# Optimization experiments

Measured on AMD Instinct MI355X. Metric: run time of the kernel, lower is better.

The kernel has to match this reference:

```python
import jax, jax.numpy as jnp
import numpy as np

N = 50000   # nodes
E = 800000  # edges (avg degree 16)
D = 256     # input = hidden = output dim
L = 3       # num_layers


def setup_inputs() -> dict:
    key = jax.random.key(0)
    k0, k1, k2, k3 = jax.random.split(key, 4)
    x = jax.random.normal(k0, (N, D), dtype=jnp.float32)
    edge_index = jax.random.randint(k1, (2, E), 0, N, dtype=jnp.int32)
    # SAGEConv params per layer: lin_l (neighbor path, with bias), lin_r (root path)
    Wl = jax.random.normal(k2, (L, D, D), dtype=jnp.float32) * 0.05
    Wr = jax.random.normal(k3, (L, D, D), dtype=jnp.float32) * 0.05
    b = jnp.zeros((L, D), dtype=jnp.float32)
    return {"x": x, "edge_index": edge_index, "Wl": Wl, "Wr": Wr, "b": b}


def reference(x, edge_index, Wl, Wr, b):
    src = edge_index[0]
    dst = edge_index[1]
    # in-degree for mean aggregation (clamped to avoid div-by-zero)
    deg = jax.ops.segment_sum(jnp.ones((E,), x.dtype), dst, num_segments=N)
    inv_deg = (1.0 / jnp.maximum(deg, 1.0))[:, None]  # [N,1]
    h = x
    for i in range(L):
        # gather source features, scatter-add into destinations, then mean
        agg = jax.ops.segment_sum(h[src], dst, num_segments=N) * inv_deg  # [N,D]
        h = agg @ Wl[i] + h @ Wr[i] + b[i]
        if i < L - 1:
            h = jax.nn.relu(h)  # dropout(p=0.1) is identity in eval mode
    return h
```

## Files before the change

### kernel.cpp

```cpp
#include <hip/hip_runtime.h>


typedef __attribute__((ext_vector_type(8))) _Float16 f16x8;
typedef __attribute__((ext_vector_type(4))) float f32x4;

__global__ void count_deg_kernel(const int* __restrict__ dst,
                                 int* __restrict__ deg, int E) {
    int i = (blockIdx.x * blockDim.x + threadIdx.x) * 2;
    if (i + 1 < E) {
        int2 d = *(const int2*)&dst[i];
        atomicAdd(&deg[d.x], 1);
        atomicAdd(&deg[d.y], 1);
    } else if (i < E) {
        atomicAdd(&deg[dst[i]], 1);
    }
}

__device__ __forceinline__ int block_excl_scan_256(int v, int tid) {
    int lane = tid & 63, w = tid >> 6;
    int x = v;
#pragma unroll
    for (int off = 1; off < 64; off <<= 1) {
        int y = __shfl_up(x, off);
        if (lane >= off) x += y;
    }
    __shared__ int wsum[4], woff[4];
    if (lane == 63) wsum[w] = x;
    __syncthreads();
    if (tid == 0) {
        int a = 0;
#pragma unroll
        for (int i = 0; i < 4; ++i) { woff[i] = a; a += wsum[i]; }
    }
    __syncthreads();
    return woff[w] + x - v;
}

__global__ void scan_phase1(const int* __restrict__ deg,
                            int* __restrict__ partial, int n) {
    int base = blockIdx.x * 1024;
    int s = 0;
    for (int i = threadIdx.x; i < 1024; i += 256) {
        int idx = base + i;
        s += (idx < n) ? deg[idx] : 0;
    }
    __shared__ int ws4[4];
    int lane = threadIdx.x & 63, w = threadIdx.x >> 6;
#pragma unroll
    for (int off = 32; off; off >>= 1) s += __shfl_down(s, off);
    if (lane == 0) ws4[w] = s;
    __syncthreads();
    if (threadIdx.x == 0)
        partial[blockIdx.x] = ws4[0] + ws4[1] + ws4[2] + ws4[3];
}

__global__ void scan_phase2(int* __restrict__ partial, int nb,
                            int* __restrict__ rowptr, int n, int E) {
    int tid = threadIdx.x;
    int v = (tid < nb) ? partial[tid] : 0;
    int ex = block_excl_scan_256(v, tid);
    if (tid < nb) partial[tid] = ex;
    if (tid == 0) rowptr[n] = E;
}

__global__ void scan_phase3(const int* __restrict__ deg,
                            const int* __restrict__ partial,
                            int* __restrict__ rowptr, int* __restrict__ cursor,
                            float* __restrict__ inv_deg, int n) {
    int base = blockIdx.x * 1024 + threadIdx.x * 4;
    int d[4];
#pragma unroll
    for (int j = 0; j < 4; ++j) {
        int idx = base + j;
        d[j] = (idx < n) ? deg[idx] : 0;
    }
    int tsum = d[0] + d[1] + d[2] + d[3];
    int ex = block_excl_scan_256(tsum, threadIdx.x);
    int run = partial[blockIdx.x] + ex;
#pragma unroll
    for (int j = 0; j < 4; ++j) {
        int idx = base + j;
        if (idx < n) {
            rowptr[idx] = run;
            cursor[idx] = run;
            inv_deg[idx] = 1.0f / (float)max(d[j], 1);
        }
        run += d[j];
    }
}

__global__ void fill_csr_kernel(const int* __restrict__ src,
                                const int* __restrict__ dst,
                                int* __restrict__ cursor,
                                int* __restrict__ csr_src, int E) {
    int i = (blockIdx.x * blockDim.x + threadIdx.x) * 2;
    if (i + 1 < E) {
        int2 d = *(const int2*)&dst[i];
        int2 s = *(const int2*)&src[i];
        int p0 = atomicAdd(&cursor[d.x], 1);
        csr_src[p0] = s.x;
        int p1 = atomicAdd(&cursor[d.y], 1);
        csr_src[p1] = s.y;
    } else if (i < E) {
        int p = atomicAdd(&cursor[dst[i]], 1);
        csr_src[p] = src[i];
    }
}

__global__ void presplit_w_kernel(const float* __restrict__ Wl,
                                  const float* __restrict__ Wr,
                                  _Float16* __restrict__ Wf,
                                  int* __restrict__ deg, int N, int total) {
    int idx = blockIdx.x * blockDim.x + threadIdx.x;
    if (idx < N) deg[idx] = 0;
    if (idx >= total) return;
    int l = idx >> 17;
    int rem = idx & 131071;
    int s = rem >> 16;
    int kc = rem & 65535;
    int k = kc >> 8, c = kc & 255;
    const float* W = s ? Wr : Wl;
    float w = W[((size_t)l * 256 + k) * 256 + c];
    int k0c = k >> 5, g = (k >> 3) & 3, j = k & 7;
    int tile = c >> 4, col = c & 15;
    int fi = (l * 2 + s) * 65536 + k0c * 8192 + ((tile * 4 + g) * 16 + col) * 8 + j;
    Wf[fi] = (_Float16)w;
}

__device__ __forceinline__ void gemm_from_lds64(
    const _Float16 (*Ah)[65][8], int tid, const _Float16* __restrict__ Wf_l,
    const float* __restrict__ bias, _Float16* __restrict__ zl,
    _Float16* __restrict__ zr, int r0, int M) {
    const int wave = tid >> 6, lane = tid & 63;
    const int l15 = lane & 15, lg = lane >> 4;
    const int wr = (wave & 1) * 32;
    const int wc = (wave >> 1) * 64;
    const int tg0 = wc >> 4;
    const _Float16* wbase = Wf_l + (lg * 16 + l15) * 8;

    f32x4 accl[2][4], accr[2][4];
#pragma unroll
    for (int rt = 0; rt < 2; ++rt)
#pragma unroll
        for (int t = 0; t < 4; ++t) {
            accl[rt][t] = (f32x4)(0.0f);
            accr[rt][t] = (f32x4)(0.0f);
        }

    f16x8 blc[4], brc[4];
#pragma unroll
    for (int t = 0; t < 4; ++t) {
        blc[t] = *(const f16x8*)&wbase[(tg0 + t) * 512];
        brc[t] = *(const f16x8*)&wbase[65536 + (tg0 + t) * 512];
    }

#pragma unroll
    for (int s = 0; s < 8; ++s) {
        f16x8 bln[4], brn[4];
        if (s < 7) {
            const _Float16* wn = wbase + (s + 1) * 8192;
#pragma unroll
            for (int t = 0; t < 4; ++t) {
                bln[t] = *(const f16x8*)&wn[(tg0 + t) * 512];
                brn[t] = *(const f16x8*)&wn[65536 + (tg0 + t) * 512];
            }
        }
        f16x8 a0 = *(const f16x8*)&Ah[s * 4 + lg][wr + l15][0];
        f16x8 a1 = *(const f16x8*)&Ah[s * 4 + lg][wr + 16 + l15][0];
#pragma unroll
        for (int t = 0; t < 4; ++t) {
            accl[0][t] = __builtin_amdgcn_mfma_f32_16x16x32_f16(a0, blc[t],
                                                                accl[0][t], 0, 0, 0);
            accl[1][t] = __builtin_amdgcn_mfma_f32_16x16x32_f16(a1, blc[t],
                                                                accl[1][t], 0, 0, 0);
            accr[0][t] = __builtin_amdgcn_mfma_f32_16x16x32_f16(a0, brc[t],
                                                                accr[0][t], 0, 0, 0);
            accr[1][t] = __builtin_amdgcn_mfma_f32_16x16x32_f16(a1, brc[t],
                                                                accr[1][t], 0, 0, 0);
        }
        if (s < 7) {
#pragma unroll
            for (int t = 0; t < 4; ++t) {
                blc[t] = bln[t];
                brc[t] = brn[t];
            }
        }
    }

    float bv[4];
#pragma unroll
    for (int t = 0; t < 4; ++t) bv[t] = bias[wc + t * 16 + l15];
#pragma unroll
    for (int rt = 0; rt < 2; ++rt) {
#pragma unroll
        for (int r = 0; r < 4; ++r) {
            int grow = r0 + wr + rt * 16 + lg * 4 + r;
            if (grow >= M) continue;
#pragma unroll
            for (int t = 0; t < 4; ++t) {
                int col = wc + t * 16 + l15;
                int p = col >> 5, off = col & 31;
                size_t zi = ((size_t)p * M + grow) * 32 + off;
                zl[zi] = (_Float16)accl[rt][t][r];
                zr[zi] = (_Float16)(accr[rt][t][r] + bv[t]);
            }
        }
    }
}

__global__ __launch_bounds__(512) void gemm_dual_kernel(
    const float* __restrict__ xsrc, const _Float16* __restrict__ hsrc,
    int f32src, _Float16* __restrict__ zl, _Float16* __restrict__ zr,
    const _Float16* __restrict__ Wf_l, const float* __restrict__ bias, int M) {
    __shared__ __align__(16) _Float16 Ah[32][65][8];
    const int tid = threadIdx.x;
    const int r0 = blockIdx.x * 64;
#pragma unroll
    for (int i = 0; i < 4; ++i) {
        int idx = i * 512 + tid;
        int row = idx >> 5, g = idx & 31;
        int grow = r0 + row;
        f16x8 v = (f16x8)(_Float16)0;
        if (grow < M) {
            if (f32src) {
                const float4* p =
                    (const float4*)&xsrc[(size_t)grow * 256 + g * 8];
                float4 v0 = p[0], v1 = p[1];
                v[0] = (_Float16)v0.x; v[1] = (_Float16)v0.y;
                v[2] = (_Float16)v0.z; v[3] = (_Float16)v0.w;
                v[4] = (_Float16)v1.x; v[5] = (_Float16)v1.y;
                v[6] = (_Float16)v1.z; v[7] = (_Float16)v1.w;
            } else {
                v = *(const f16x8*)&hsrc[(size_t)grow * 256 + g * 8];
            }
        }
        *(f16x8*)&Ah[g][row][0] = v;
    }
    __syncthreads();
    gemm_from_lds64(Ah, tid, Wf_l, bias, zl, zr, r0, M);
}

__global__ __launch_bounds__(256) void combine_panel_kernel(
    const _Float16* __restrict__ zl, const _Float16* __restrict__ zr,
    const int* __restrict__ rowptr, const int* __restrict__ csr_src,
    const float* __restrict__ inv_deg, _Float16* __restrict__ hout,
    float* __restrict__ fout, int n, int mode) {
    const int slice = blockIdx.x & 7;
    const int chunk = blockIdx.x >> 3;
    const int grp = threadIdx.x >> 2;
    const int l4 = threadIdx.x & 3;
    const _Float16* zlp = zl + (size_t)slice * n * 32 + l4 * 8;
    const _Float16* zrp = zr + (size_t)slice * n * 32 + l4 * 8;

#pragma unroll
    for (int i = 0; i < 4; ++i) {
        int v = chunk * 256 + i * 64 + grp;
        if (v >= n) continue;
        int beg = rowptr[v], end = rowptr[v + 1];
        float acc[8] = {0.f, 0.f, 0.f, 0.f, 0.f, 0.f, 0.f, 0.f};
        for (int e = beg; e < end; e += 8) {
            f16x8 t[8];
#pragma unroll
            for (int k = 0; k < 8; ++k) {
                int ee = min(e + k, end - 1);
                int u = csr_src[ee];
                t[k] = *(const f16x8*)&zlp[(size_t)u * 32];
            }
#pragma unroll
            for (int k = 0; k < 8; ++k) {
                if (e + k < end) {
#pragma unroll
                    for (int j = 0; j < 8; ++j) acc[j] += (float)t[k][j];
                }
            }
        }
        float sc = inv_deg[v];
        f16x8 zp = *(const f16x8*)&zrp[(size_t)v * 32];
        float o[8];
#pragma unroll
        for (int j = 0; j < 8; ++j) o[j] = acc[j] * sc + (float)zp[j];
        int cbase = slice * 32 + l4 * 8;
        if (mode == 0) {
            f16x8 hv;
#pragma unroll
            for (int j = 0; j < 8; ++j) hv[j] = (_Float16)fmaxf(o[j], 0.0f);
            *(f16x8*)&hout[(size_t)v * 256 + cbase] = hv;
        } else {
            float4* op = (float4*)&fout[(size_t)v * 256 + cbase];
            op[0] = make_float4(o[0], o[1], o[2], o[3]);
            op[1] = make_float4(o[4], o[5], o[6], o[7]);
        }
    }
}

extern "C" void kernel_launch(void* const* d_in, const int* in_sizes, int n_in,
                              void* d_out, int out_size, void* d_ws, size_t ws_size,
                              hipStream_t stream) {
    const int D = 256;
    const int N = in_sizes[0] / D;
    const int E = in_sizes[1] / 2;
    const int L = in_sizes[2] / (D * D);

    const float* x  = (const float*)d_in[0];
    const int*   ei = (const int*)d_in[1];
    const float* Wl = (const float*)d_in[2];
    const float* Wr = (const float*)d_in[3];
    const float* b  = (const float*)d_in[4];
    const int* src = ei;
    const int* dst = ei + E;

    size_t off = 0;
    auto alloc = [&](size_t bytes) {
        void* p = (char*)d_ws + off;
        off += (bytes + 255) & ~(size_t)255;
        return p;
    };
    int*   deg     = (int*)alloc((size_t)N * 4);
    int*   rowptr  = (int*)alloc((size_t)(N + 1) * 4);
    int*   cursor  = (int*)alloc((size_t)N * 4);
    float* inv_deg = (float*)alloc((size_t)N * 4);
    int*   csr_src = (int*)alloc((size_t)E * 4);
    int*   partial = (int*)alloc(256 * 4);
    _Float16* zlP  = (_Float16*)alloc((size_t)N * D * 2);
    _Float16* zrP  = (_Float16*)alloc((size_t)N * D * 2);
    _Float16* hbuf = (_Float16*)alloc((size_t)N * D * 2);
    _Float16* Wf   = (_Float16*)alloc((size_t)L * 2 * 65536 * 2);
    (void)ws_size;

    _Float16* zlQ = (_Float16*)d_out;
    _Float16* zrQ = zlQ + (size_t)N * D;
    float* outf = (float*)d_out;

    const int scan_blocks = (N + 1023) / 1024;

    int wtotal = L * 2 * 65536;
    hipLaunchKernelGGL(presplit_w_kernel, dim3((wtotal + 255) / 256), dim3(256),
                       0, stream, Wl, Wr, Wf, deg, N, wtotal);

    hipLaunchKernelGGL(count_deg_kernel, dim3((E / 2 + 255) / 256), dim3(256),
                       0, stream, dst, deg, E);
    hipLaunchKernelGGL(scan_phase1, dim3(scan_blocks), dim3(256), 0, stream,
                       deg, partial, N);
    hipLaunchKernelGGL(scan_phase2, dim3(1), dim3(256), 0, stream,
                       partial, scan_blocks, rowptr, N, E);
    hipLaunchKernelGGL(scan_phase3, dim3(scan_blocks), dim3(256), 0, stream,
                       deg, partial, rowptr, cursor, inv_deg, N);
    hipLaunchKernelGGL(fill_csr_kernel, dim3((E / 2 + 255) / 256), dim3(256),
                       0, stream, src, dst, cursor, csr_src, E);

    const int gemm_blocks = (N + 63) / 64;
    const int comb_blocks = 8 * ((N + 255) / 256);

    hipLaunchKernelGGL(gemm_dual_kernel, dim3(gemm_blocks), dim3(512), 0,
                       stream, x, (const _Float16*)nullptr, 1, zlP, zrP,
                       Wf, b, N);
    hipLaunchKernelGGL(combine_panel_kernel, dim3(comb_blocks), dim3(256), 0,
                       stream, zlP, zrP, rowptr, csr_src, inv_deg,
                       hbuf, outf, N, 0);
    hipLaunchKernelGGL(gemm_dual_kernel, dim3(gemm_blocks), dim3(512), 0,
                       stream, (const float*)nullptr, hbuf, 0, zlQ, zrQ,
                       Wf + 131072, b + D, N);
    hipLaunchKernelGGL(combine_panel_kernel, dim3(comb_blocks), dim3(256), 0,
                       stream, zlQ, zrQ, rowptr, csr_src, inv_deg,
                       hbuf, outf, N, 0);
    hipLaunchKernelGGL(gemm_dual_kernel, dim3(gemm_blocks), dim3(512), 0,
                       stream, (const float*)nullptr, hbuf, 0, zlP, zrP,
                       Wf + 262144, b + 2 * D, N);
    hipLaunchKernelGGL(combine_panel_kernel, dim3(comb_blocks), dim3(256), 0,
                       stream, zlP, zrP, rowptr, csr_src, inv_deg,
                       hbuf, outf, N, 1);
}
```

Before: 391.6 us.

## Sort nodes by degree bucket for balanced aggregation and widen gather unroll

Adds a counting-sort pass (histogram, scan, scatter) that orders nodes by in-degree, and the combine kernel walks nodes through this permutation so neighbouring threads have similar degrees. This is meant to cut wavefront divergence from uneven neighbour loop trip counts. The gather unroll also grows from 8 to 16 outstanding loads per iteration for more memory-level parallelism. The cost is three extra small launches, an extra indirection, scattered output writes and more registers.

```diff
diff --git a/kernel.cpp b/kernel.cpp
--- a/kernel.cpp
+++ b/kernel.cpp
@@ -107,12 +107,43 @@
     }
 }
 
+__global__ void bucket_hist_kernel(const int* __restrict__ deg,
+                                   int* __restrict__ hist, int n) {
+    int i = blockIdx.x * blockDim.x + threadIdx.x;
+    if (i < n) atomicAdd(&hist[min(deg[i], 63)], 1);
+}
+
+__global__ void bucket_scan_kernel(int* __restrict__ hist) {
+    int tid = threadIdx.x;
+    int v = hist[tid];
+    int x = v;
+#pragma unroll
+    for (int off = 1; off < 64; off <<= 1) {
+        int y = __shfl_up(x, off);
+        if (tid >= off) x += y;
+    }
+    hist[tid] = x - v;
+}
+
+__global__ void bucket_scatter_kernel(const int* __restrict__ deg,
+                                      int* __restrict__ hist,
+                                      int* __restrict__ perm, int n) {
+    int i = blockIdx.x * blockDim.x + threadIdx.x;
+    if (i < n) {
+        int b = min(deg[i], 63);
+        int p = atomicAdd(&hist[b], 1);
+        perm[p] = i;
+    }
+}
+
 __global__ void presplit_w_kernel(const float* __restrict__ Wl,
                                   const float* __restrict__ Wr,
                                   _Float16* __restrict__ Wf,
-                                  int* __restrict__ deg, int N, int total) {
+                                  int* __restrict__ deg, int* __restrict__ hist,
+                                  int N, int total) {
     int idx = blockIdx.x * blockDim.x + threadIdx.x;
     if (idx < N) deg[idx] = 0;
+    if (idx < 64) hist[idx] = 0;
     if (idx >= total) return;
     int l = idx >> 17;
     int rem = idx & 131071;
@@ -243,8 +274,8 @@
 __global__ __launch_bounds__(256) void combine_panel_kernel(
     const _Float16* __restrict__ zl, const _Float16* __restrict__ zr,
     const int* __restrict__ rowptr, const int* __restrict__ csr_src,
-    const float* __restrict__ inv_deg, _Float16* __restrict__ hout,
-    float* __restrict__ fout, int n, int mode) {
+    const float* __restrict__ inv_deg, const int* __restrict__ perm,
+    _Float16* __restrict__ hout, float* __restrict__ fout, int n, int mode) {
     const int slice = blockIdx.x & 7;
     const int chunk = blockIdx.x >> 3;
     const int grp = threadIdx.x >> 2;
@@ -254,28 +285,29 @@
 
 #pragma unroll
     for (int i = 0; i < 4; ++i) {
-        int v = chunk * 256 + i * 64 + grp;
-        if (v >= n) continue;
+        int idx = chunk * 256 + i * 64 + grp;
+        if (idx >= n) continue;
+        int v = perm[idx];
         int beg = rowptr[v], end = rowptr[v + 1];
+        float sc = inv_deg[v];
+        f16x8 zp = *(const f16x8*)&zrp[(size_t)v * 32];
         float acc[8] = {0.f, 0.f, 0.f, 0.f, 0.f, 0.f, 0.f, 0.f};
-        for (int e = beg; e < end; e += 8) {
-            f16x8 t[8];
-#pragma unroll
-            for (int k = 0; k < 8; ++k) {
+        for (int e = beg; e < end; e += 16) {
+            f16x8 t[16];
+#pragma unroll
+            for (int k = 0; k < 16; ++k) {
                 int ee = min(e + k, end - 1);
                 int u = csr_src[ee];
                 t[k] = *(const f16x8*)&zlp[(size_t)u * 32];
             }
 #pragma unroll
-            for (int k = 0; k < 8; ++k) {
+            for (int k = 0; k < 16; ++k) {
                 if (e + k < end) {
 #pragma unroll
                     for (int j = 0; j < 8; ++j) acc[j] += (float)t[k][j];
                 }
             }
         }
-        float sc = inv_deg[v];
-        f16x8 zp = *(const f16x8*)&zrp[(size_t)v * 32];
         float o[8];
 #pragma unroll
         for (int j = 0; j < 8; ++j) o[j] = acc[j] * sc + (float)zp[j];
@@ -321,6 +353,8 @@
     float* inv_deg = (float*)alloc((size_t)N * 4);
     int*   csr_src = (int*)alloc((size_t)E * 4);
     int*   partial = (int*)alloc(256 * 4);
+    int*   hist    = (int*)alloc(64 * 4);
+    int*   perm    = (int*)alloc((size_t)N * 4);
     _Float16* zlP  = (_Float16*)alloc((size_t)N * D * 2);
     _Float16* zrP  = (_Float16*)alloc((size_t)N * D * 2);
     _Float16* hbuf = (_Float16*)alloc((size_t)N * D * 2);
@@ -332,10 +366,11 @@
     float* outf = (float*)d_out;
 
     const int scan_blocks = (N + 1023) / 1024;
+    const int nthr_blocks = (N + 255) / 256;
 
     int wtotal = L * 2 * 65536;
     hipLaunchKernelGGL(presplit_w_kernel, dim3((wtotal + 255) / 256), dim3(256),
-                       0, stream, Wl, Wr, Wf, deg, N, wtotal);
+                       0, stream, Wl, Wr, Wf, deg, hist, N, wtotal);
 
     hipLaunchKernelGGL(count_deg_kernel, dim3((E / 2 + 255) / 256), dim3(256),
                        0, stream, dst, deg, E);
@@ -348,6 +383,12 @@
     hipLaunchKernelGGL(fill_csr_kernel, dim3((E / 2 + 255) / 256), dim3(256),
                        0, stream, src, dst, cursor, csr_src, E);
 
+    hipLaunchKernelGGL(bucket_hist_kernel, dim3(nthr_blocks), dim3(256), 0,
+                       stream, deg, hist, N);
+    hipLaunchKernelGGL(bucket_scan_kernel, dim3(1), dim3(64), 0, stream, hist);
+    hipLaunchKernelGGL(bucket_scatter_kernel, dim3(nthr_blocks), dim3(256), 0,
+                       stream, deg, hist, perm, N);
+
     const int gemm_blocks = (N + 63) / 64;
     const int comb_blocks = 8 * ((N + 255) / 256);
 
@@ -355,18 +396,18 @@
                        stream, x, (const _Float16*)nullptr, 1, zlP, zrP,
                        Wf, b, N);
     hipLaunchKernelGGL(combine_panel_kernel, dim3(comb_blocks), dim3(256), 0,
-                       stream, zlP, zrP, rowptr, csr_src, inv_deg,
+                       stream, zlP, zrP, rowptr, csr_src, inv_deg, perm,
                        hbuf, outf, N, 0);
     hipLaunchKernelGGL(gemm_dual_kernel, dim3(gemm_blocks), dim3(512), 0,
                        stream, (const float*)nullptr, hbuf, 0, zlQ, zrQ,
                        Wf + 131072, b + D, N);
     hipLaunchKernelGGL(combine_panel_kernel, dim3(comb_blocks), dim3(256), 0,
-                       stream, zlQ, zrQ, rowptr, csr_src, inv_deg,
+                       stream, zlQ, zrQ, rowptr, csr_src, inv_deg, perm,
                        hbuf, outf, N, 0);
     hipLaunchKernelGGL(gemm_dual_kernel, dim3(gemm_blocks), dim3(512), 0,
                        stream, (const float*)nullptr, hbuf, 0, zlP, zrP,
                        Wf + 262144, b + 2 * D, N);
     hipLaunchKernelGGL(combine_panel_kernel, dim3(comb_blocks), dim3(256), 0,
-                       stream, zlP, zrP, rowptr, csr_src, inv_deg,
+                       stream, zlP, zrP, rowptr, csr_src, inv_deg, perm,
                        hbuf, outf, N, 1);
 }
```

After: 708.6 us. +80.9%, slower.
